# Kernel optimization log

Measured on AMD Instinct MI355X. Metric: run time of the kernel, lower is better.

Reference implementation:

```python
import jax, jax.numpy as jnp
import numpy as np

C_IN = 128
C_HID = 32
N_HEADS = 4
INF = 1e9
N = 384


def setup_inputs() -> dict:
    key = jax.random.key(0)
    ks = jax.random.split(key, 10)
    d = {}
    d["x"] = jax.random.normal(ks[0], (1, N, N, C_IN), dtype=jnp.float32)
    d["mask"] = jnp.ones((1, N, N), dtype=jnp.float32)
    # LayerNorm params
    d["ln_gamma"] = jnp.ones((C_IN,), dtype=jnp.float32)
    d["ln_beta"] = jnp.zeros((C_IN,), dtype=jnp.float32)
    # triangle-bias projection (no bias): [H, C]
    d["w_bias"] = jax.random.normal(ks[1], (N_HEADS, C_IN), dtype=jnp.float32) * 0.02
    # q/k/v projections (no bias): [H, Dh, C]
    s = 1.0 / np.sqrt(C_IN)
    d["wq"] = jax.random.normal(ks[2], (N_HEADS, C_HID, C_IN), dtype=jnp.float32) * s
    d["wk"] = jax.random.normal(ks[3], (N_HEADS, C_HID, C_IN), dtype=jnp.float32) * s
    d["wv"] = jax.random.normal(ks[4], (N_HEADS, C_HID, C_IN), dtype=jnp.float32) * s
    # gating linear (with bias): [H, Dh, C], [H, Dh]
    d["wg"] = jax.random.normal(ks[5], (N_HEADS, C_HID, C_IN), dtype=jnp.float32) * s
    d["bg"] = jnp.ones((N_HEADS, C_HID), dtype=jnp.float32)
    # output linear: [C, H*Dh], [C]
    d["wo"] = jax.random.normal(ks[6], (C_IN, N_HEADS * C_HID), dtype=jnp.float32) * (1.0 / np.sqrt(N_HEADS * C_HID))
    d["bo"] = jnp.zeros((C_IN,), dtype=jnp.float32)
    return d


def reference(x, mask, ln_gamma, ln_beta, w_bias, wq, wk, wv, wg, bg, wo, bo):
    # starting=True -> no transpose
    # LayerNorm over last dim
    mu = jnp.mean(x, axis=-1, keepdims=True)
    var = jnp.var(x, axis=-1, keepdims=True)
    xn = (x - mu) * jax.lax.rsqrt(var + 1e-5) * ln_gamma + ln_beta  # [B,I,J,C]

    # triangle bias: [B,H,I,J] -> broadcast over row dim of scores
    tri_bias = jnp.einsum("bijc,hc->bhij", xn, w_bias)
    # mask bias: [B,I,1,1,J]
    mask_bias = (mask - 1.0)[:, :, None, None, :] * INF

    scale = 1.0 / np.sqrt(C_HID)
    q = jnp.einsum("bijc,hdc->bijhd", xn, wq) * scale  # [B,I,J,H,Dh]
    k = jnp.einsum("bijc,hdc->bijhd", xn, wk)
    v = jnp.einsum("bijc,hdc->bijhd", xn, wv)

    # scores over keys j' within each row i: [B,I,H,J,J]
    scores = jnp.einsum("biqhd,bikhd->bihqk", q, k)
    scores = scores + tri_bias[:, None, :, :, :] + mask_bias
    a = jax.nn.softmax(scores, axis=-1)

    o = jnp.einsum("bihqk,bikhd->biqhd", a, v)  # [B,I,J,H,Dh]

    g = jax.nn.sigmoid(jnp.einsum("bijc,hdc->bijhd", xn, wg) + bg)
    o = o * g
    o = o.reshape(*o.shape[:-2], N_HEADS * C_HID)
    out = jnp.einsum("bijk,ck->bijc", o, wo) + bo  # [B,I,J,C]
    return out
```

## Files before the change

### kernel.cpp

```cpp
#include <hip/hip_runtime.h>

#define Nn 384
#define Cc 128
#define DHh 32
#define NHh 4
#define NPOS (Nn*Nn)
#define LOG2E 1.4426950408889634f

typedef unsigned short ushort_t;
typedef __attribute__((ext_vector_type(8))) short bf16x8;
typedef __attribute__((ext_vector_type(4))) float f32x4;
typedef __attribute__((ext_vector_type(16))) float f32x16;
typedef __attribute__((ext_vector_type(2))) int i32x2;
typedef __attribute__((ext_vector_type(4))) int i32x4;

__device__ __forceinline__ ushort_t f2bf(float f) {
  union { float f; unsigned int u; } v; v.f = f;
  unsigned int r = v.u + 0x7fffu + ((v.u >> 16) & 1u);
  return (ushort_t)(r >> 16);
}
__device__ __forceinline__ float bf2f(ushort_t u) {
  union { unsigned int u; float f; } v; v.u = ((unsigned int)u) << 16;
  return v.f;
}
__device__ __forceinline__ int cvt_pk_bf16(float a, float b) {
  int r;
  asm("v_cvt_pk_bf16_f32 %0, %1, %2" : "=v"(r) : "v"(a), "v"(b));
  return r;
}

__global__ __launch_bounds__(256) void k_wt(const float* __restrict__ wq,
    const float* __restrict__ wk, const float* __restrict__ wv,
    const float* __restrict__ wg, const float* __restrict__ wo,
    ushort_t* __restrict__ wBt, ushort_t* __restrict__ woT) {
  for (int rep = 0; rep < 4; ++rep) {
    int idx = blockIdx.x * 256 + threadIdx.x + rep * 20480;
    if (idx < 65536) {
      int c = idx >> 7, k = idx & 127;
      int mat = c >> 7, row = c & 127;
      const float* src;
      float scale = 1.0f;
      if (mat == 0)      { src = wq; scale = 0.17677669529663687f * LOG2E; }
      else if (mat == 1) { src = wk; }
      else if (mat == 2) { src = wv; }
      else               { src = wg; }
      wBt[idx] = f2bf(src[row * 128 + k] * scale);
    } else {
      int j = idx - 65536;
      woT[j] = f2bf(wo[j]);
    }
  }
}

__global__ __launch_bounds__(256) void k_ln(const float* __restrict__ x,
    const float* __restrict__ gamma, const float* __restrict__ beta,
    const float* __restrict__ wb, const float* __restrict__ mask,
    unsigned int* __restrict__ xnb, float* __restrict__ bias3,
    float* __restrict__ mb_ws) {
  int wid = threadIdx.x >> 6, lane = threadIdx.x & 63;
  int p = blockIdx.x * 4 + wid;
  int i = p / Nn, j = p - i * Nn;
  size_t base = (size_t)p * Cc + lane * 2;
  float2 xv = *(const float2*)&x[base];
  float s = xv.x + xv.y;
  #pragma unroll
  for (int off = 1; off < 64; off <<= 1) s += __shfl_xor(s, off, 64);
  float mu = s * (1.0f / Cc);
  float d0 = xv.x - mu, d1 = xv.y - mu;
  float sq = d0 * d0 + d1 * d1;
  #pragma unroll
  for (int off = 1; off < 64; off <<= 1) sq += __shfl_xor(sq, off, 64);
  float rs = rsqrtf(sq * (1.0f / Cc) + 1e-5f);
  float2 g2 = *(const float2*)&gamma[lane * 2];
  float2 b2 = *(const float2*)&beta[lane * 2];
  float xn0 = d0 * rs * g2.x + b2.x;
  float xn1 = d1 * rs * g2.y + b2.y;
  unsigned int pack = (unsigned int)f2bf(xn0) | ((unsigned int)f2bf(xn1) << 16);
  xnb[(size_t)p * 64 + lane] = pack;
  #pragma unroll
  for (int h = 0; h < NHh; ++h) {
    float2 w2 = *(const float2*)&wb[h * Cc + lane * 2];
    float t = xn0 * w2.x + xn1 * w2.y;
    #pragma unroll
    for (int off = 1; off < 64; off <<= 1) t += __shfl_xor(t, off, 64);
    if (lane == 0)
      bias3[(size_t)h * NPOS + (size_t)(j >> 2) * (Nn * 4) + i * 4 + (j & 3)] =
          t * LOG2E;
  }
  if (lane == 1) mb_ws[p] = (mask[p] - 1.0f) * (1e9f * LOG2E);
}

__global__ __launch_bounds__(256, 3) void k_proj(const ushort_t* __restrict__ xnb,
    const ushort_t* __restrict__ wBt, const float* __restrict__ bg,
    ushort_t* __restrict__ qkvg) {
  __shared__ __align__(16) char plds[34816 + 18432];
  ushort_t* As = (ushort_t*)plds;
  ushort_t* Bs = (ushort_t*)(plds + 34816);
  ushort_t* Cs = (ushort_t*)(plds + 34816);
  const int tid = threadIdx.x, lane = tid & 63, w = tid >> 6;
  const int q15 = lane & 15, quad = lane >> 4;
  const int m0 = blockIdx.x * 128;

  #pragma unroll
  for (int r = 0; r < 8; ++r) {
    int idx = tid + 256 * r;
    int row = idx >> 4, seg = idx & 15;
    *(uint4*)&As[row * 136 + seg * 8] =
        *(const uint4*)&xnb[(size_t)(m0 + row) * 128 + seg * 8];
  }
  __syncthreads();
  bf16x8 af[4][2];
  #pragma unroll
  for (int kk = 0; kk < 4; ++kk)
    #pragma unroll
    for (int mi = 0; mi < 2; ++mi)
      af[kk][mi] = *(const bf16x8*)&As[(w * 32 + mi * 16 + q15) * 136 +
                                       kk * 32 + quad * 8];

  for (int nb = 0; nb < 8; ++nb) {
    #pragma unroll
    for (int r = 0; r < 4; ++r) {
      int idx = tid + 256 * r;
      int row = idx >> 4, seg = idx & 15;
      *(uint4*)&Bs[row * 136 + seg * 8] =
          *(const uint4*)&wBt[(size_t)(nb * 64 + row) * 128 + seg * 8];
    }
    __syncthreads();

    f32x4 acc[2][4];
    #pragma unroll
    for (int mi = 0; mi < 2; ++mi)
      #pragma unroll
      for (int ni = 0; ni < 4; ++ni) {
        float init = 0.0f;
        if (nb >= 6) init = bg[(nb & 1) * 64 + ni * 16 + q15];
        acc[mi][ni][0] = init; acc[mi][ni][1] = init;
        acc[mi][ni][2] = init; acc[mi][ni][3] = init;
      }
    #pragma unroll
    for (int kk = 0; kk < 4; ++kk) {
      bf16x8 bf[4];
      #pragma unroll
      for (int ni = 0; ni < 4; ++ni)
        bf[ni] = *(const bf16x8*)&Bs[(ni * 16 + q15) * 136 + kk * 32 + quad * 8];
      #pragma unroll
      for (int mi = 0; mi < 2; ++mi)
        #pragma unroll
        for (int ni = 0; ni < 4; ++ni)
          acc[mi][ni] = __builtin_amdgcn_mfma_f32_16x16x32_bf16(
              af[kk][mi], bf[ni], acc[mi][ni], 0, 0, 0);
    }
    __syncthreads();
    #pragma unroll
    for (int mi = 0; mi < 2; ++mi)
      #pragma unroll
      for (int ni = 0; ni < 4; ++ni)
        #pragma unroll
        for (int r = 0; r < 4; ++r) {
          int rowL = w * 32 + mi * 16 + quad * 4 + r;
          Cs[rowL * 72 + ni * 16 + q15] = f2bf(acc[mi][ni][r]);
        }
    __syncthreads();
    const int mat = nb >> 1;
    #pragma unroll
    for (int r = 0; r < 4; ++r) {
      int idx = tid + 256 * r;
      int row = idx >> 3, seg = idx & 7;
      int cl = (nb & 1) * 64 + seg * 8;
      int hh = cl >> 5, dd = cl & 31;
      uint4 v = *(const uint4*)&Cs[row * 72 + seg * 8];
      *(uint4*)&qkvg[(size_t)mat * (NHh * (size_t)NPOS * 32) +
                     (size_t)hh * ((size_t)NPOS * 32) +
                     (size_t)(m0 + row) * 32 + dd] = v;
    }
    __syncthreads();
  }
}

__global__ __launch_bounds__(256, 4) void k_attn(const ushort_t* __restrict__ qkvg,
    const float* __restrict__ bias3, const float* __restrict__ mb_ws,
    ushort_t* __restrict__ o_ws) {
  __shared__ __align__(16) char lds[33280];
  ushort_t* KsB = (ushort_t*)lds;
  ushort_t* VtB = (ushort_t*)(lds + 16384);
  float*  lsmem = (float*)(lds + 32768);

  const int tid = threadIdx.x, lane = tid & 63, w = tid >> 6;
  const int ql = lane & 31, h5 = lane >> 5;
  const int h  = blockIdx.x / 3;
  const int qt = blockIdx.x % 3;
  const int i  = blockIdx.y;
  const int q0 = qt * 128;

  const ushort_t* q_all = qkvg;
  const ushort_t* k_all = qkvg + (size_t)1 * NHh * NPOS * 32;
  const ushort_t* v_all = qkvg + (size_t)2 * NHh * NPOS * 32;
  const ushort_t* g_all = qkvg + (size_t)3 * NHh * NPOS * 32;
  const size_t hbase = ((size_t)h * NPOS + (size_t)i * Nn) * 32;
  const float* brow = bias3 + (size_t)h * NPOS;
  const float* mrow = mb_ws + (size_t)i * Nn;

  const int qglob = q0 + w * 32 + ql;
  const ushort_t* qp = q_all + hbase + (size_t)qglob * 32;
  const bf16x8 qf0 = *(const bf16x8*)&qp[h5 * 8];
  const bf16x8 qf1 = *(const bf16x8*)&qp[16 + h5 * 8];

  f32x16 oacc;
  #pragma unroll
  for (int r = 0; r < 16; ++r) oacc[r] = 0.f;
  float lsum = 0.f;

  const int swk = (ql >> 1) & 3;
  const int swv = (ql >> 1) & 7;

  for (int ch = 0; ch < 3; ++ch) {
    const int kbase = ch * 128;
    ushort_t* Ksb = KsB + (ch & 1) * 4096;
    ushort_t* Vtb = VtB + (ch & 1) * 4096;
    #pragma unroll
    for (int r = 0; r < 2; ++r) {
      int idx = tid + 256 * r;
      int row = idx >> 2, seg = idx & 3;
      *(uint4*)&Ksb[row * 32 + (seg ^ ((row >> 1) & 3)) * 8] =
          *(const uint4*)&k_all[hbase + (size_t)(kbase + row) * 32 + seg * 8];
    }
    #pragma unroll
    for (int r = 0; r < 4; ++r) {
      int idx = tid + 256 * r;
      int dp = idx & 15, kp = idx >> 4;
      unsigned int a0 = *(const unsigned int*)
          &v_all[hbase + (size_t)(kbase + 2 * kp) * 32 + dp * 2];
      unsigned int a1 = *(const unsigned int*)
          &v_all[hbase + (size_t)(kbase + 2 * kp + 1) * 32 + dp * 2];
      unsigned int lo = (a0 & 0xffffu) | (a1 << 16);
      unsigned int hi = (a0 >> 16) | (a1 & 0xffff0000u);
      unsigned int* v32 = (unsigned int*)Vtb;
      int col = ((kp >> 2) ^ (dp & 7)) * 4 + (kp & 3);
      v32[(2 * dp) * 64 + col] = lo;
      v32[(2 * dp + 1) * 64 + col] = hi;
    }
    __syncthreads();

    #pragma unroll
    for (int t = 0; t < 4; ++t) {
      bf16x8 kf0 = *(const bf16x8*)&Ksb[(t * 32 + ql) * 32 + ((h5)     ^ swk) * 8];
      bf16x8 kf1 = *(const bf16x8*)&Ksb[(t * 32 + ql) * 32 + ((2 + h5) ^ swk) * 8];
      const int K0 = kbase + t * 32 + 4 * h5;
      f32x16 acc;
      #pragma unroll
      for (int g = 0; g < 4; ++g) {
        f32x4 b4 = *(const f32x4*)
            &brow[(size_t)((K0 >> 2) + 2 * g) * (Nn * 4) + qglob * 4];
        f32x4 m4 = *(const f32x4*)&mrow[K0 + 8 * g];
        acc[4 * g + 0] = b4[0] + m4[0];
        acc[4 * g + 1] = b4[1] + m4[1];
        acc[4 * g + 2] = b4[2] + m4[2];
        acc[4 * g + 3] = b4[3] + m4[3];
      }
      acc = __builtin_amdgcn_mfma_f32_32x32x16_bf16(kf0, qf0, acc, 0, 0, 0);
      acc = __builtin_amdgcn_mfma_f32_32x32x16_bf16(kf1, qf1, acc, 0, 0, 0);
      int pk[8];
      #pragma unroll
      for (int r = 0; r < 16; r += 2) {
        float e0 = exp2f(acc[r]);
        float e1 = exp2f(acc[r + 1]);
        lsum += e0 + e1;
        pk[r >> 1] = cvt_pk_bf16(e0, e1);
      }
      #pragma unroll
      for (int b2 = 0; b2 < 2; ++b2) {
        i32x2 s0 = __builtin_amdgcn_permlane32_swap(pk[4 * b2 + 0],
                                                    pk[4 * b2 + 2], false, false);
        i32x2 s1 = __builtin_amdgcn_permlane32_swap(pk[4 * b2 + 1],
                                                    pk[4 * b2 + 3], false, false);
        union { i32x4 i; bf16x8 b; } pu;
        pu.i[0] = s0[0]; pu.i[1] = s1[0]; pu.i[2] = s0[1]; pu.i[3] = s1[1];
        int kt = 2 * t + b2;
        bf16x8 vb = *(const bf16x8*)
            &Vtb[ql * 128 + ((2 * kt + h5) ^ swv) * 8];
        oacc = __builtin_amdgcn_mfma_f32_32x32x16_bf16(pu.b, vb, oacc, 0, 0, 0);
      }
    }
  }

  float lsf = lsum + __shfl_xor(lsum, 32, 64);
  if (lane < 32) lsmem[w * 32 + ql] = lsf;
  float inv[16];
  #pragma unroll
  for (int g = 0; g < 4; ++g) {
    f32x4 lv = *(const f32x4*)&lsmem[w * 32 + g * 8 + 4 * h5];
    #pragma unroll
    for (int j = 0; j < 4; ++j) inv[g * 4 + j] = 1.0f / lv[j];
  }
  #pragma unroll
  for (int r = 0; r < 16; ++r) {
    int qloc = w * 32 + (r & 3) + 8 * (r >> 2) + 4 * h5;
    int posg = i * Nn + q0 + qloc;
    float gpre = bf2f(g_all[((size_t)h * NPOS + posg) * 32 + ql]);
    float gate = 1.0f / (1.0f + __expf(-gpre));
    o_ws[(size_t)posg * Cc + h * DHh + ql] = f2bf(oacc[r] * inv[r] * gate);
  }
}

__global__ __launch_bounds__(256, 2) void k_out(const ushort_t* __restrict__ o_ws,
    const ushort_t* __restrict__ woT, const float* __restrict__ bo,
    float* __restrict__ out) {
  __shared__ ushort_t As[128 * 136];
  __shared__ ushort_t Bs[128 * 136];
  const int tid = threadIdx.x, lane = tid & 63, w = tid >> 6;
  const int q15 = lane & 15, quad = lane >> 4;
  const size_t m0 = (size_t)blockIdx.x * 128;

  #pragma unroll
  for (int r = 0; r < 8; ++r) {
    int idx = tid + 256 * r;
    int row = idx >> 4, seg = idx & 15;
    *(uint4*)&As[row * 136 + seg * 8] =
        *(const uint4*)&o_ws[(m0 + row) * 128 + seg * 8];
    *(uint4*)&Bs[row * 136 + seg * 8] =
        *(const uint4*)&woT[(size_t)row * 128 + seg * 8];
  }
  __syncthreads();

  f32x4 acc[2][8];
  #pragma unroll
  for (int mi = 0; mi < 2; ++mi)
    #pragma unroll
    for (int ni = 0; ni < 8; ++ni) {
      acc[mi][ni][0] = 0.f; acc[mi][ni][1] = 0.f;
      acc[mi][ni][2] = 0.f; acc[mi][ni][3] = 0.f;
    }
  #pragma unroll
  for (int kk = 0; kk < 4; ++kk) {
    bf16x8 a_[2];
    #pragma unroll
    for (int mi = 0; mi < 2; ++mi)
      a_[mi] = *(const bf16x8*)&As[(w * 32 + mi * 16 + q15) * 136 +
                                   kk * 32 + quad * 8];
    #pragma unroll
    for (int ni = 0; ni < 8; ++ni) {
      bf16x8 b_ = *(const bf16x8*)&Bs[(ni * 16 + q15) * 136 + kk * 32 + quad * 8];
      #pragma unroll
      for (int mi = 0; mi < 2; ++mi)
        acc[mi][ni] = __builtin_amdgcn_mfma_f32_16x16x32_bf16(
            a_[mi], b_, acc[mi][ni], 0, 0, 0);
    }
  }
  #pragma unroll
  for (int ni = 0; ni < 8; ++ni) {
    float bov = bo[ni * 16 + q15];
    #pragma unroll
    for (int mi = 0; mi < 2; ++mi)
      #pragma unroll
      for (int r = 0; r < 4; ++r) {
        int rowL = w * 32 + mi * 16 + quad * 4 + r;
        out[(m0 + rowL) * Cc + ni * 16 + q15] = acc[mi][ni][r] + bov;
      }
  }
}

extern "C" void kernel_launch(void* const* d_in, const int* in_sizes, int n_in,
                              void* d_out, int out_size, void* d_ws, size_t ws_size,
                              hipStream_t stream) {
  const float* x     = (const float*)d_in[0];
  const float* mask  = (const float*)d_in[1];
  const float* gamma = (const float*)d_in[2];
  const float* beta  = (const float*)d_in[3];
  const float* wb    = (const float*)d_in[4];
  const float* wq    = (const float*)d_in[5];
  const float* wk    = (const float*)d_in[6];
  const float* wv    = (const float*)d_in[7];
  const float* wg    = (const float*)d_in[8];
  const float* bg    = (const float*)d_in[9];
  const float* wo    = (const float*)d_in[10];
  const float* bo    = (const float*)d_in[11];
  float* out = (float*)d_out;

  char* ws = (char*)d_ws;
  ushort_t* xnb   = (ushort_t*)ws;
  ushort_t* qkvg  = (ushort_t*)(ws + (size_t)NPOS * 128 * 2);
  float*    bias3 = (float*)(ws + (size_t)NPOS * 128 * 2
                                + (size_t)4 * NHh * NPOS * 32 * 2);
  ushort_t* wBt   = (ushort_t*)((char*)bias3 + (size_t)NHh * NPOS * 4);
  ushort_t* woT   = wBt + 65536;
  float*    mb_ws = (float*)(woT + 16384);
  ushort_t* o_ws  = xnb;

  hipLaunchKernelGGL(k_wt, dim3(80), dim3(256), 0, stream,
                     wq, wk, wv, wg, wo, wBt, woT);
  hipLaunchKernelGGL(k_ln, dim3(NPOS / 4), dim3(256), 0, stream,
                     x, gamma, beta, wb, mask, (unsigned int*)xnb, bias3, mb_ws);
  hipLaunchKernelGGL(k_proj, dim3(NPOS / 128), dim3(256), 0, stream,
                     xnb, wBt, bg, qkvg);
  hipLaunchKernelGGL(k_attn, dim3(12, Nn), dim3(256), 0, stream,
                     qkvg, bias3, mb_ws, o_ws);
  hipLaunchKernelGGL(k_out, dim3(NPOS / 128), dim3(256), 0, stream,
                     o_ws, woT, bo, out);
}
```

Before: 386.1 us.

## Software-pipeline K/V and bias global loads in attention kernel with register prefetch

Fully unrolls the three key chunks and issues the global loads for the next K/V chunk into registers before computing on the current chunk, writing them to LDS afterwards. Triangle-bias loads are prefetched one tile ahead so their latency overlaps the MFMA and exp work. The row-sum scratch area now reuses part of the V buffer, which shrinks LDS use. This raises register pressure under the 4-blocks-per-CU launch bound.

```diff
diff --git a/kernel.cpp b/kernel.cpp
--- a/kernel.cpp
+++ b/kernel.cpp
@@ -180,10 +180,10 @@
 __global__ __launch_bounds__(256, 4) void k_attn(const ushort_t* __restrict__ qkvg,
     const float* __restrict__ bias3, const float* __restrict__ mb_ws,
     ushort_t* __restrict__ o_ws) {
-  __shared__ __align__(16) char lds[33280];
+  __shared__ __align__(16) char lds[32768];
   ushort_t* KsB = (ushort_t*)lds;
   ushort_t* VtB = (ushort_t*)(lds + 16384);
-  float*  lsmem = (float*)(lds + 32768);
+  float*  lsmem = (float*)(lds + 24576);
 
   const int tid = threadIdx.x, lane = tid & 63, w = tid >> 6;
   const int ql = lane & 31, h5 = lane >> 5;
@@ -197,91 +197,129 @@
   const ushort_t* v_all = qkvg + (size_t)2 * NHh * NPOS * 32;
   const ushort_t* g_all = qkvg + (size_t)3 * NHh * NPOS * 32;
   const size_t hbase = ((size_t)h * NPOS + (size_t)i * Nn) * 32;
-  const float* brow = bias3 + (size_t)h * NPOS;
-  const float* mrow = mb_ws + (size_t)i * Nn;
-
   const int qglob = q0 + w * 32 + ql;
+
+  const float* bptr = bias3 + (size_t)h * NPOS + (size_t)h5 * (Nn * 4) + qglob * 4;
+  const float* mptr = mb_ws + (size_t)i * Nn + 4 * h5;
+
   const ushort_t* qp = q_all + hbase + (size_t)qglob * 32;
   const bf16x8 qf0 = *(const bf16x8*)&qp[h5 * 8];
   const bf16x8 qf1 = *(const bf16x8*)&qp[16 + h5 * 8];
 
+  const int krow0 = tid >> 2, kseg = tid & 3;
+  const int vdp = tid & 15, vkp0 = tid >> 4;
+
   f32x16 oacc;
   #pragma unroll
   for (int r = 0; r < 16; ++r) oacc[r] = 0.f;
   float lsum = 0.f;
-
   const int swk = (ql >> 1) & 3;
   const int swv = (ql >> 1) & 7;
 
-  for (int ch = 0; ch < 3; ++ch) {
-    const int kbase = ch * 128;
-    ushort_t* Ksb = KsB + (ch & 1) * 4096;
-    ushort_t* Vtb = VtB + (ch & 1) * 4096;
-    #pragma unroll
-    for (int r = 0; r < 2; ++r) {
-      int idx = tid + 256 * r;
-      int row = idx >> 2, seg = idx & 3;
-      *(uint4*)&Ksb[row * 32 + (seg ^ ((row >> 1) & 3)) * 8] =
-          *(const uint4*)&k_all[hbase + (size_t)(kbase + row) * 32 + seg * 8];
-    }
-    #pragma unroll
-    for (int r = 0; r < 4; ++r) {
-      int idx = tid + 256 * r;
-      int dp = idx & 15, kp = idx >> 4;
-      unsigned int a0 = *(const unsigned int*)
-          &v_all[hbase + (size_t)(kbase + 2 * kp) * 32 + dp * 2];
-      unsigned int a1 = *(const unsigned int*)
-          &v_all[hbase + (size_t)(kbase + 2 * kp + 1) * 32 + dp * 2];
-      unsigned int lo = (a0 & 0xffffu) | (a1 << 16);
-      unsigned int hi = (a0 >> 16) | (a1 & 0xffff0000u);
-      unsigned int* v32 = (unsigned int*)Vtb;
-      int col = ((kp >> 2) ^ (dp & 7)) * 4 + (kp & 3);
-      v32[(2 * dp) * 64 + col] = lo;
-      v32[(2 * dp + 1) * 64 + col] = hi;
-    }
-    __syncthreads();
-
-    #pragma unroll
-    for (int t = 0; t < 4; ++t) {
-      bf16x8 kf0 = *(const bf16x8*)&Ksb[(t * 32 + ql) * 32 + ((h5)     ^ swk) * 8];
-      bf16x8 kf1 = *(const bf16x8*)&Ksb[(t * 32 + ql) * 32 + ((2 + h5) ^ swk) * 8];
-      const int K0 = kbase + t * 32 + 4 * h5;
-      f32x16 acc;
-      #pragma unroll
-      for (int g = 0; g < 4; ++g) {
-        f32x4 b4 = *(const f32x4*)
-            &brow[(size_t)((K0 >> 2) + 2 * g) * (Nn * 4) + qglob * 4];
-        f32x4 m4 = *(const f32x4*)&mrow[K0 + 8 * g];
-        acc[4 * g + 0] = b4[0] + m4[0];
-        acc[4 * g + 1] = b4[1] + m4[1];
-        acc[4 * g + 2] = b4[2] + m4[2];
-        acc[4 * g + 3] = b4[3] + m4[3];
-      }
-      acc = __builtin_amdgcn_mfma_f32_32x32x16_bf16(kf0, qf0, acc, 0, 0, 0);
-      acc = __builtin_amdgcn_mfma_f32_32x32x16_bf16(kf1, qf1, acc, 0, 0, 0);
-      int pk[8];
-      #pragma unroll
-      for (int r = 0; r < 16; r += 2) {
-        float e0 = exp2f(acc[r]);
-        float e1 = exp2f(acc[r + 1]);
-        lsum += e0 + e1;
-        pk[r >> 1] = cvt_pk_bf16(e0, e1);
-      }
-      #pragma unroll
-      for (int b2 = 0; b2 < 2; ++b2) {
-        i32x2 s0 = __builtin_amdgcn_permlane32_swap(pk[4 * b2 + 0],
-                                                    pk[4 * b2 + 2], false, false);
-        i32x2 s1 = __builtin_amdgcn_permlane32_swap(pk[4 * b2 + 1],
-                                                    pk[4 * b2 + 3], false, false);
-        union { i32x4 i; bf16x8 b; } pu;
-        pu.i[0] = s0[0]; pu.i[1] = s1[0]; pu.i[2] = s0[1]; pu.i[3] = s1[1];
-        int kt = 2 * t + b2;
-        bf16x8 vb = *(const bf16x8*)
-            &Vtb[ql * 128 + ((2 * kt + h5) ^ swv) * 8];
-        oacc = __builtin_amdgcn_mfma_f32_32x32x16_bf16(pu.b, vb, oacc, 0, 0, 0);
-      }
-    }
-  }
+  uint4 kv0, kv1;
+  unsigned int va[8];
+  f32x4 bb0, bb1, bb2, bb3;
+
+#define KV_ISSUE(CH) do {                                                     \
+    const size_t kb = hbase + (size_t)((CH) * 128) * 32;                      \
+    kv0 = *(const uint4*)&k_all[kb + (size_t)krow0 * 32 + kseg * 8];          \
+    kv1 = *(const uint4*)&k_all[kb + (size_t)(krow0 + 64) * 32 + kseg * 8];   \
+    _Pragma("unroll")                                                         \
+    for (int r = 0; r < 4; ++r) {                                             \
+      va[2*r+0] = *(const unsigned int*)                                      \
+          &v_all[kb + (size_t)(vkp0 + 16*r) * 64 + vdp * 2];                  \
+      va[2*r+1] = *(const unsigned int*)                                      \
+          &v_all[kb + (size_t)(vkp0 + 16*r) * 64 + 32 + vdp * 2];             \
+    }                                                                         \
+  } while (0)
+
+#define KV_WRITE(CH) do {                                                     \
+    ushort_t* Ksb_ = KsB + ((CH) & 1) * 4096;                                 \
+    unsigned int* v32_ = (unsigned int*)(VtB + ((CH) & 1) * 4096);            \
+    *(uint4*)&Ksb_[krow0 * 32 + (kseg ^ ((krow0 >> 1) & 3)) * 8] = kv0;       \
+    *(uint4*)&Ksb_[(krow0 + 64) * 32 +                                        \
+                   (kseg ^ (((krow0 + 64) >> 1) & 3)) * 8] = kv1;             \
+    _Pragma("unroll")                                                         \
+    for (int r = 0; r < 4; ++r) {                                             \
+      int kp_ = vkp0 + 16 * r;                                                \
+      unsigned int a0 = va[2*r], a1 = va[2*r+1];                              \
+      unsigned int lo = (a0 & 0xffffu) | (a1 << 16);                          \
+      unsigned int hi = (a0 >> 16) | (a1 & 0xffff0000u);                      \
+      int col_ = ((kp_ >> 2) ^ (vdp & 7)) * 4 + (kp_ & 3);                    \
+      v32_[(2 * vdp) * 64 + col_] = lo;                                       \
+      v32_[(2 * vdp + 1) * 64 + col_] = hi;                                   \
+    }                                                                         \
+  } while (0)
+
+#define BIAS_LOAD(CH, T) do {                                                 \
+    bb0 = *(const f32x4*)&bptr[((CH) * 32 + (T) * 8 + 0) * (Nn * 4)];         \
+    bb1 = *(const f32x4*)&bptr[((CH) * 32 + (T) * 8 + 2) * (Nn * 4)];         \
+    bb2 = *(const f32x4*)&bptr[((CH) * 32 + (T) * 8 + 4) * (Nn * 4)];         \
+    bb3 = *(const f32x4*)&bptr[((CH) * 32 + (T) * 8 + 6) * (Nn * 4)];         \
+  } while (0)
+
+#define TILE(CH, T, PF, NCH, NT) do {                                         \
+    ushort_t* Ksb_ = KsB + ((CH) & 1) * 4096;                                 \
+    ushort_t* Vtb_ = VtB + ((CH) & 1) * 4096;                                 \
+    bf16x8 kf0 = *(const bf16x8*)                                             \
+        &Ksb_[((T) * 32 + ql) * 32 + ((0 + h5) ^ swk) * 8];                   \
+    bf16x8 kf1 = *(const bf16x8*)                                             \
+        &Ksb_[((T) * 32 + ql) * 32 + ((2 + h5) ^ swk) * 8];                   \
+    f32x4 m0_ = *(const f32x4*)&mptr[(CH) * 128 + (T) * 32 + 0];              \
+    f32x4 m1_ = *(const f32x4*)&mptr[(CH) * 128 + (T) * 32 + 8];              \
+    f32x4 m2_ = *(const f32x4*)&mptr[(CH) * 128 + (T) * 32 + 16];             \
+    f32x4 m3_ = *(const f32x4*)&mptr[(CH) * 128 + (T) * 32 + 24];             \
+    f32x16 acc;                                                               \
+    _Pragma("unroll")                                                         \
+    for (int j = 0; j < 4; ++j) {                                             \
+      acc[0  + j] = bb0[j] + m0_[j];                                          \
+      acc[4  + j] = bb1[j] + m1_[j];                                          \
+      acc[8  + j] = bb2[j] + m2_[j];                                          \
+      acc[12 + j] = bb3[j] + m3_[j];                                          \
+    }                                                                         \
+    if (PF) BIAS_LOAD(NCH, NT);                \
+    acc = __builtin_amdgcn_mfma_f32_32x32x16_bf16(kf0, qf0, acc, 0, 0, 0);    \
+    acc = __builtin_amdgcn_mfma_f32_32x32x16_bf16(kf1, qf1, acc, 0, 0, 0);    \
+    int pk[8];                                                                \
+    _Pragma("unroll")                                                         \
+    for (int r = 0; r < 16; r += 2) {                                         \
+      float e0 = exp2f(acc[r]);                                               \
+      float e1 = exp2f(acc[r + 1]);                                           \
+      lsum += e0 + e1;                                                        \
+      pk[r >> 1] = cvt_pk_bf16(e0, e1);                                       \
+    }                                                                         \
+    _Pragma("unroll")                                                         \
+    for (int b2 = 0; b2 < 2; ++b2) {                                          \
+      i32x2 s0 = __builtin_amdgcn_permlane32_swap(pk[4*b2+0], pk[4*b2+2],     \
+                                                  false, false);              \
+      i32x2 s1 = __builtin_amdgcn_permlane32_swap(pk[4*b2+1], pk[4*b2+3],     \
+                                                  false, false);              \
+      union { i32x4 i; bf16x8 b; } pu;                                        \
+      pu.i[0] = s0[0]; pu.i[1] = s1[0]; pu.i[2] = s0[1]; pu.i[3] = s1[1];     \
+      bf16x8 vb = *(const bf16x8*)                                            \
+          &Vtb_[ql * 128 + ((2 * (2*(T)+b2) + h5) ^ swv) * 8];                \
+      oacc = __builtin_amdgcn_mfma_f32_32x32x16_bf16(pu.b, vb, oacc, 0,0,0);  \
+    }                                                                         \
+  } while (0)
+
+  KV_ISSUE(0);
+  BIAS_LOAD(0, 0);
+  KV_WRITE(0);
+  KV_ISSUE(1);
+  __syncthreads();
+  TILE(0,0, 1, 0,1); TILE(0,1, 1, 0,2); TILE(0,2, 1, 0,3); TILE(0,3, 1, 1,0);
+  KV_WRITE(1);
+  KV_ISSUE(2);
+  __syncthreads();
+  TILE(1,0, 1, 1,1); TILE(1,1, 1, 1,2); TILE(1,2, 1, 1,3); TILE(1,3, 1, 2,0);
+  KV_WRITE(2);
+  __syncthreads();
+  TILE(2,0, 1, 2,1); TILE(2,1, 1, 2,2); TILE(2,2, 1, 2,3); TILE(2,3, 0, 0,0);
+
+#undef KV_ISSUE
+#undef KV_WRITE
+#undef BIAS_LOAD
+#undef TILE
 
   float lsf = lsum + __shfl_xor(lsum, 32, 64);
   if (lane < 32) lsmem[w * 32 + ql] = lsf;
```

Measured after the change: 372.6 us. -3.5%, faster.
